# Performance work log

Measured on AMD Instinct MI355X. Metric: run time of the kernel, lower is better.

Reference implementation:

```python
import jax, jax.numpy as jnp
import numpy as np

B, N, C = 16, 32768, 3
PRE, POST, IOU_THRESH = 4096, 512, 0.7


def setup_inputs() -> dict:
    key = jax.random.key(0)
    k1, k2, k3, k4 = jax.random.split(key, 4)
    centers = jax.random.uniform(k1, (B, N, 3), minval=0.0, maxval=70.0)
    sizes = jax.random.uniform(k2, (B, N, 3), minval=1.0, maxval=5.0)
    ry = jax.random.uniform(k3, (B, N, 1), minval=-np.pi, maxval=np.pi)
    batch_box_preds = jnp.concatenate([centers, sizes, ry], axis=-1)  # (B,N,7)
    batch_cls_preds = jax.random.uniform(k4, (B, N, C))  # normalized class scores
    return {"batch_box_preds": batch_box_preds, "batch_cls_preds": batch_cls_preds}


def _nms_single(boxes, scores):
    """Greedy class-agnostic NMS for one sample.
    boxes: (N,7) [x,y,z,dx,dy,dz,ry]; scores: (N,).
    Returns selected indices into the original N boxes and a validity mask,
    both of fixed length POST (padded).
    BEV IoU uses axis-aligned footprints (x,y,dx,dy)."""
    top_s, top_i = jax.lax.top_k(scores, PRE)  # pre-maxsize filtering by score
    tb = boxes[top_i]  # (PRE,7)
    x1 = tb[:, 0] - tb[:, 3] * 0.5
    x2 = tb[:, 0] + tb[:, 3] * 0.5
    y1 = tb[:, 1] - tb[:, 4] * 0.5
    y2 = tb[:, 1] + tb[:, 4] * 0.5
    area = (x2 - x1) * (y2 - y1)

    def step(active, _):
        ms = jnp.where(active, top_s, -jnp.inf)
        j = jnp.argmax(ms)
        valid = active[j]
        ix = jnp.clip(jnp.minimum(x2, x2[j]) - jnp.maximum(x1, x1[j]), 0.0)
        iy = jnp.clip(jnp.minimum(y2, y2[j]) - jnp.maximum(y1, y1[j]), 0.0)
        inter = ix * iy
        iou = inter / (area + area[j] - inter + 1e-8)
        # suppress overlapping boxes (j suppresses itself, iou==1)
        active = active & jnp.where(valid, iou < IOU_THRESH, True)
        return active, (jnp.where(valid, top_i[j], 0), valid)

    active0 = jnp.ones(PRE, dtype=bool)
    _, (sel_idx, sel_valid) = jax.lax.scan(step, active0, None, length=POST)
    return sel_idx, sel_valid


def reference(batch_box_preds, batch_cls_preds):
    # cur_roi_scores, cur_roi_labels = torch.max(cls_preds, dim=1)
    scores = jnp.max(batch_cls_preds, axis=-1)          # (B,N)
    labels = jnp.argmax(batch_cls_preds, axis=-1)       # (B,N)
    sel_idx, sel_valid = jax.vmap(_nms_single)(batch_box_preds, scores)  # (B,POST)
    gather = jax.vmap(lambda a, i: a[i])
    rois = jnp.where(sel_valid[..., None], gather(batch_box_preds, sel_idx), 0.0)  # (B,POST,7)
    roi_scores = jnp.where(sel_valid, gather(scores, sel_idx), 0.0)                # (B,POST)
    roi_labels = jnp.where(sel_valid, gather(labels, sel_idx), 0) + 1              # (B,POST), pad -> 1 as in torch code
    return rois, roi_scores, roi_labels
```

## Files before the change

### kernel.cpp

```cpp
#include <hip/hip_runtime.h>
#include <stdint.h>

#define BATCH 16
#define NBOX  32768
#define PRE   4096
#define POST  512

#define PADIDX(i) ((i) + ((i) >> 4))

typedef unsigned long long u64;
typedef unsigned int u32;

__device__ inline u64 shfl64(u64 v, int src) {
    int lo = __shfl((int)(v & 0xffffffffULL), src);
    int hi = __shfl((int)(v >> 32), src);
    return ((u64)(u32)hi << 32) | (u32)lo;
}

__global__ __launch_bounds__(1024) void k_sortkeys4096(const float* __restrict__ cls,
                                                       u64* __restrict__ out) {
    __shared__ u64 s[PRE + (PRE >> 4)];
    int g = blockIdx.x;
    u64* dst = out + (size_t)g * PRE;
    int tid = threadIdx.x;
    for (int i = tid; i < PRE; i += 1024) {
        int idx = g * PRE + i;
        const float* c = cls + (size_t)idx * 3;
        float sc = fmaxf(fmaxf(c[0], c[1]), c[2]);
        u32 sb = __float_as_uint(sc);
        s[PADIDX(i)] = ((u64)(~sb) << 32) | (u32)(idx & (NBOX - 1));
    }
    for (int k = 2; k <= PRE; k <<= 1) {
        for (int jj = k >> 1; jj > 0; jj >>= 1) {
            __syncthreads();
            for (int p = tid; p < PRE / 2; p += 1024) {
                int i = 2 * p - (p & (jj - 1));
                int l = i + jj;
                bool asc = ((i & k) == 0);
                u64 a = s[PADIDX(i)], b = s[PADIDX(l)];
                if ((a > b) == asc) { s[PADIDX(i)] = b; s[PADIDX(l)] = a; }
            }
        }
    }
    __syncthreads();
    for (int i = tid; i < PRE; i += 1024) dst[i] = s[PADIDX(i)];
}

__global__ __launch_bounds__(256) void k_mergepath(const u64* __restrict__ in,
                                                   u64* __restrict__ out, int npairs) {
    __shared__ u64 sA[PRE], sB[PRE];
    int b = blockIdx.x / npairs, p = blockIdx.x % npairs;
    const u64* A  = in + ((size_t)b * npairs * 2 + (size_t)p * 2) * PRE;
    const u64* Bp = A + PRE;
    u64* dst = out + ((size_t)b * npairs + p) * PRE;
    int tid = threadIdx.x;
    for (int i = tid; i < PRE; i += 256) { sA[i] = A[i]; sB[i] = Bp[i]; }
    __syncthreads();
    int d = tid * 16;
    int lo = d > PRE ? d - PRE : 0;
    int hi = d < PRE ? d : PRE;
    while (lo < hi) {
        int mid = (lo + hi) >> 1;
        if (sA[mid] < sB[d - 1 - mid]) lo = mid + 1; else hi = mid;
    }
    int a = lo, bi = d - lo;
    u64 av = a  < PRE ? sA[a]  : ~0ULL;
    u64 bv = bi < PRE ? sB[bi] : ~0ULL;
    u64 res[16];
    #pragma unroll
    for (int q = 0; q < 16; ++q) {
        bool ta = av < bv;
        res[q] = ta ? av : bv;
        if (ta) { ++a;  av = a  < PRE ? sA[a]  : ~0ULL; }
        else    { ++bi; bv = bi < PRE ? sB[bi] : ~0ULL; }
    }
    #pragma unroll
    for (int q = 0; q < 16; ++q) dst[d + q] = res[q];
}

__global__ __launch_bounds__(256) void k_coords(const u64* __restrict__ topkeys,
                                                const float* __restrict__ boxes,
                                                float* __restrict__ cx1,
                                                float* __restrict__ cy1,
                                                float* __restrict__ cx2,
                                                float* __restrict__ cy2,
                                                float* __restrict__ car,
                                                u64* __restrict__ flags) {
    int g = blockIdx.x * 256 + threadIdx.x;
    if (g < BATCH * 64) flags[g] = 0ULL;
    int b = g >> 12;
    u64 key = topkeys[g];
    int n = (int)(key & 0xffffffffULL);
    const float* bp = boxes + ((size_t)b * NBOX + n) * 7;
    float cx = bp[0], cy = bp[1], dx = bp[3], dy = bp[4];
    float hx = __fmul_rn(dx, 0.5f), hy = __fmul_rn(dy, 0.5f);
    float x1 = __fsub_rn(cx, hx), x2 = __fadd_rn(cx, hx);
    float y1 = __fsub_rn(cy, hy), y2 = __fadd_rn(cy, hy);
    cx1[g] = x1; cy1[g] = y1; cx2[g] = x2; cy2[g] = y2;
    car[g] = __fmul_rn(__fsub_rn(x2, x1), __fsub_rn(y2, y1));
}

__global__ __launch_bounds__(256) void k_iou(const float* __restrict__ cx1,
                                             const float* __restrict__ cy1,
                                             const float* __restrict__ cx2,
                                             const float* __restrict__ cy2,
                                             const float* __restrict__ car,
                                             u64* __restrict__ maskp,
                                             u64* __restrict__ flags) {
    __shared__ float s1[64], s2[64], s3[64], s4[64], s5[64];
    int b = blockIdx.y;
    int t = blockIdx.x, blk = 0;
    while (t >= 64 - blk) { t -= 64 - blk; ++blk; }
    int wd = blk + t;
    bool diag = (wd == blk);
    size_t base = (size_t)b * PRE;
    int tid = threadIdx.x;
    if (tid < 64) {
        int i = blk * 64 + tid;
        s1[tid] = cx1[base + i]; s2[tid] = cy1[base + i];
        s3[tid] = cx2[base + i]; s4[tid] = cy2[base + i];
        s5[tid] = car[base + i];
    }
    __syncthreads();
    int w = tid >> 6, lane = tid & 63;
    int j = wd * 64 + lane;
    float jx1 = cx1[base + j], jy1 = cy1[base + j];
    float jx2 = cx2[base + j], jy2 = cy2[base + j];
    float ja  = car[base + j];
    const double M = (double)0.7f - 0x1p-25;
    u64 wavebits = 0;
    int r0 = w * 16;
    #pragma unroll 4
    for (int r = 0; r < 16; ++r) {
        int i = blk * 64 + r0 + r;
        float rx1 = s1[r0 + r], ry1 = s2[r0 + r];
        float rx2 = s3[r0 + r], ry2 = s4[r0 + r], ra = s5[r0 + r];
        float ix = fmaxf(__fsub_rn(fminf(jx2, rx2), fmaxf(jx1, rx1)), 0.0f);
        float iy = fmaxf(__fsub_rn(fminf(jy2, ry2), fmaxf(jy1, ry1)), 0.0f);
        float inter = __fmul_rn(ix, iy);
        bool cand = (inter > 0.0f) && (!diag || j > i);
        u64 m = 0;
        if (__ballot(cand)) {
            float ssum = __fadd_rn(ja, ra);
            float d    = __fsub_rn(ssum, inter);
            float q    = __fadd_rn(d, 1e-8f);
            bool sup = cand && ((double)inter > M * (double)q);
            m = __ballot(sup);
        }
        if (lane == 0) maskp[((base + i) << 6) + wd] = m;
        if (m) wavebits |= 1ULL << (r0 + r);
    }
    if (lane == 0 && wavebits)
        atomicOr((unsigned long long*)&flags[b * 64 + blk], wavebits);
}

__global__ __launch_bounds__(256) void k_walk(const u64* __restrict__ maskp,
                                              const u64* __restrict__ flagbits,
                                              const u64* __restrict__ topkeys,
                                              const float* __restrict__ boxes,
                                              const float* __restrict__ cls,
                                              float* __restrict__ out) {
    __shared__ int ssel[POST];
    __shared__ int scnt;
    int b = blockIdx.x;
    int tid = threadIdx.x;
    const u64* keys = topkeys + (size_t)b * PRE;

    if (tid < 64) {
        int lane = tid;
        u64 act = ~0ULL;
        u64 nzf = flagbits[b * 64 + lane];
        int cnt = 0;
        while (true) {
            u64 bal = __ballot(act != 0ULL);
            if (!bal) break;
            int fw = __ffsll(bal) - 1;
            u64 wsel = shfl64(act, fw);
            int i = (fw << 6) + __ffsll(wsel) - 1;
            if (lane == 0) ssel[cnt] = i;
            cnt++;
            if (cnt == POST) break;
            if (lane == fw) act &= ~(1ULL << (i & 63));
            u64 fword = shfl64(nzf, fw);
            if ((fword >> (i & 63)) & 1ULL) {
                u64 row = maskp[(((size_t)b * PRE + i) << 6) + lane];
                if (lane >= fw) act &= ~row;
            }
        }
        if (lane == 0) scnt = cnt;
    }
    __syncthreads();
    int cnt = scnt;
    for (int k = tid; k < POST; k += 256) if (k >= cnt) ssel[k] = -1;
    __syncthreads();

    const int R1 = BATCH * POST * 7;
    const int R2 = R1 + BATCH * POST;
    for (int k = tid; k < POST; k += 256) {
        int j = ssel[k];
        float* ro = out + ((size_t)b * POST + k) * 7;
        float score = 0.0f, labelf = 1.0f;
        if (j >= 0) {
            u64 key = keys[j];
            int n = (int)(key & 0xffffffffULL);
            const float* bp = boxes + ((size_t)b * NBOX + n) * 7;
            #pragma unroll
            for (int c = 0; c < 7; ++c) ro[c] = bp[c];
            score = __uint_as_float(~(u32)(key >> 32));
            const float* cp = cls + ((size_t)b * NBOX + n) * 3;
            float c0 = cp[0], c1 = cp[1], c2 = cp[2];
            int lab = 0; float best = c0;
            if (c1 > best) { best = c1; lab = 1; }
            if (c2 > best) { lab = 2; }
            labelf = (float)(lab + 1);
        } else {
            #pragma unroll
            for (int c = 0; c < 7; ++c) ro[c] = 0.0f;
        }
        out[R1 + b * POST + k] = score;
        out[R2 + b * POST + k] = labelf;
    }
}

__global__ __launch_bounds__(1024) void k_nms(const u64* __restrict__ topkeys,
                                              const float* __restrict__ boxes,
                                              const float* __restrict__ cls,
                                              float* __restrict__ out) {
    __shared__ float sx1[PRE], sy1[PRE], sx2[PRE], sy2[PRE], sarea[PRE];
    __shared__ int   sorig[PRE];
    __shared__ u64   smask[PRE / 64];
    __shared__ int   ssel[POST];
    __shared__ int   scur;
    int b = blockIdx.x;
    int tid = threadIdx.x;
    const u64* keys = topkeys + (size_t)b * PRE;

    for (int i = tid; i < PRE; i += 1024) {
        u64 key = keys[i];
        int n = (int)(key & 0xffffffffULL);
        sorig[i] = n;
        const float* bp = boxes + ((size_t)b * NBOX + n) * 7;
        float cx = bp[0], cy = bp[1], dx = bp[3], dy = bp[4];
        float hx = __fmul_rn(dx, 0.5f), hy = __fmul_rn(dy, 0.5f);
        float x1 = __fsub_rn(cx, hx), x2 = __fadd_rn(cx, hx);
        float y1 = __fsub_rn(cy, hy), y2 = __fadd_rn(cy, hy);
        sx1[i] = x1; sx2[i] = x2; sy1[i] = y1; sy2[i] = y2;
        sarea[i] = __fmul_rn(__fsub_rn(x2, x1), __fsub_rn(y2, y1));
    }
    if (tid < PRE / 64) smask[tid] = ~0ULL;
    __syncthreads();

    int lane = tid & 63;
    int wv   = tid >> 6;
    for (int r = 0; r < POST; ++r) {
        if (tid < 64) {
            u64 w = smask[lane];
            u64 nz = __ballot(w != 0ULL);
            int j = -1;
            if (nz) {
                int fw = __ffsll(nz) - 1;
                u64 wf = shfl64(w, fw);
                j = (fw << 6) + __ffsll(wf) - 1;
            }
            if (lane == 0) { scur = j; ssel[r] = j; }
        }
        __syncthreads();
        int j = scur;
        if (j < 0) {
            for (int k = r + tid; k < POST; k += 1024) ssel[k] = -1;
            __syncthreads();
            break;
        }
        float x1j = sx1[j], x2j = sx2[j], y1j = sy1[j], y2j = sy2[j], aj = sarea[j];
        for (int wd = wv * 4; wd < wv * 4 + 4; ++wd) {
            u64 m = smask[wd];
            if (m == 0ULL) continue;
            int i = (wd << 6) + lane;
            float ix = fmaxf(__fsub_rn(fminf(sx2[i], x2j), fmaxf(sx1[i], x1j)), 0.0f);
            float iy = fmaxf(__fsub_rn(fminf(sy2[i], y2j), fmaxf(sy1[i], y1j)), 0.0f);
            float inter = __fmul_rn(ix, iy);
            float denom = __fadd_rn(__fsub_rn(__fadd_rn(sarea[i], aj), inter), 1e-8f);
            float iou = __fdiv_rn(inter, denom);
            u64 clr = __ballot(!(iou < 0.7f));
            if (lane == 0) smask[wd] = m & ~clr;
        }
        __syncthreads();
    }

    const int R1 = BATCH * POST * 7;
    const int R2 = R1 + BATCH * POST;
    for (int k = tid; k < POST; k += 1024) {
        int j = ssel[k];
        float* ro = out + ((size_t)b * POST + k) * 7;
        float score = 0.0f, labelf = 1.0f;
        if (j >= 0) {
            int n = sorig[j];
            const float* bp = boxes + ((size_t)b * NBOX + n) * 7;
            #pragma unroll
            for (int c = 0; c < 7; ++c) ro[c] = bp[c];
            u64 key = keys[j];
            score = __uint_as_float(~(u32)(key >> 32));
            const float* cp = cls + ((size_t)b * NBOX + n) * 3;
            float c0 = cp[0], c1 = cp[1], c2 = cp[2];
            int lab = 0; float best = c0;
            if (c1 > best) { best = c1; lab = 1; }
            if (c2 > best) { lab = 2; }
            labelf = (float)(lab + 1);
        } else {
            #pragma unroll
            for (int c = 0; c < 7; ++c) ro[c] = 0.0f;
        }
        out[R1 + b * POST + k] = score;
        out[R2 + b * POST + k] = labelf;
    }
}

extern "C" void kernel_launch(void* const* d_in, const int* in_sizes, int n_in,
                              void* d_out, int out_size, void* d_ws, size_t ws_size,
                              hipStream_t stream) {
    const float* boxes = (const float*)d_in[0];
    const float* cls   = (const float*)d_in[1];
    float* out = (float*)d_out;

    char* ws = (char*)d_ws;
    u64*   keysA = (u64*)(ws + 0);
    u64*   keysB = (u64*)(ws + 4194304);
    float* cx1   = (float*)(ws + 8388608);
    float* cy1   = (float*)(ws + 8650752);
    float* cx2   = (float*)(ws + 8912896);
    float* cy2   = (float*)(ws + 9175040);
    float* car   = (float*)(ws + 9437184);
    u64*   flags = (u64*)(ws + 9699328);
    u64*   maskp = (u64*)(ws + 9707520);
    const size_t NEED = 9707520 + (size_t)BATCH * PRE * 64 * 8;

    k_sortkeys4096<<<BATCH * 8, 1024, 0, stream>>>(cls, keysB);
    k_mergepath<<<BATCH * 4, 256, 0, stream>>>(keysB, keysA, 4);
    k_mergepath<<<BATCH * 2, 256, 0, stream>>>(keysA, keysB, 2);
    k_mergepath<<<BATCH, 256, 0, stream>>>(keysB, keysA, 1);

    if (ws_size >= NEED) {
        k_coords<<<(BATCH * PRE) / 256, 256, 0, stream>>>(keysA, boxes,
                                                          cx1, cy1, cx2, cy2, car, flags);
        k_iou<<<dim3(2080, BATCH), 256, 0, stream>>>(cx1, cy1, cx2, cy2, car,
                                                     maskp, flags);
        k_walk<<<BATCH, 256, 0, stream>>>(maskp, flags, keysA, boxes, cls, out);
    } else {
        k_nms<<<BATCH, 1024, 0, stream>>>(keysA, boxes, cls, out);
    }
}
```

Measured before the change: 328.3 us.

## Replace dense NMS suppression bitmask with sparse per-row adjacency lists

The IoU kernel no longer writes a dense 64-word bitmask row per box. It appends each suppressed index to a compact per-box list of up to 7 u16 entries, with a global spill buffer for overflow, using atomics. The walk kernel loads these lists into shared memory and rebuilds each lane's 64-bit suppression word from them. This cuts the 32 MB mask write and the dependent global reads in the serial walk. In exchange it adds atomic contention, a memset, a large shared-memory footprint, and a linear spill scan for rows with many overlaps.

Result: faster. 310.6 us (-5.4%).

```diff
diff --git a/kernel.cpp b/kernel.cpp
--- a/kernel.cpp
+++ b/kernel.cpp
@@ -10,6 +10,7 @@
 
 typedef unsigned long long u64;
 typedef unsigned int u32;
+typedef unsigned short u16;
 
 __device__ inline u64 shfl64(u64 v, int src) {
     int lo = __shfl((int)(v & 0xffffffffULL), src);
@@ -84,10 +85,8 @@
                                                 float* __restrict__ cy1,
                                                 float* __restrict__ cx2,
                                                 float* __restrict__ cy2,
-                                                float* __restrict__ car,
-                                                u64* __restrict__ flags) {
+                                                float* __restrict__ car) {
     int g = blockIdx.x * 256 + threadIdx.x;
-    if (g < BATCH * 64) flags[g] = 0ULL;
     int b = g >> 12;
     u64 key = topkeys[g];
     int n = (int)(key & 0xffffffffULL);
@@ -105,15 +104,17 @@
                                              const float* __restrict__ cx2,
                                              const float* __restrict__ cy2,
                                              const float* __restrict__ car,
-                                             u64* __restrict__ maskp,
-                                             u64* __restrict__ flags) {
+                                             u32* __restrict__ counts,
+                                             u16* __restrict__ lists,
+                                             u32* __restrict__ spcnt,
+                                             u32* __restrict__ spill) {
     __shared__ float s1[64], s2[64], s3[64], s4[64], s5[64];
     int b = blockIdx.y;
     int t = blockIdx.x, blk = 0;
     while (t >= 64 - blk) { t -= 64 - blk; ++blk; }
     int wd = blk + t;
-    bool diag = (wd == blk);
     size_t base = (size_t)b * PRE;
+    int bb = b * PRE;
     int tid = threadIdx.x;
     if (tid < 64) {
         int i = blk * 64 + tid;
@@ -128,7 +129,6 @@
     float jx2 = cx2[base + j], jy2 = cy2[base + j];
     float ja  = car[base + j];
     const double M = (double)0.7f - 0x1p-25;
-    u64 wavebits = 0;
     int r0 = w * 16;
     #pragma unroll 4
     for (int r = 0; r < 16; ++r) {
@@ -138,7 +138,7 @@
         float ix = fmaxf(__fsub_rn(fminf(jx2, rx2), fmaxf(jx1, rx1)), 0.0f);
         float iy = fmaxf(__fsub_rn(fminf(jy2, ry2), fmaxf(jy1, ry1)), 0.0f);
         float inter = __fmul_rn(ix, iy);
-        bool cand = (inter > 0.0f) && (!diag || j > i);
+        bool cand = (j > i) && (inter > 0.0f);
         u64 m = 0;
         if (__ballot(cand)) {
             float ssum = __fadd_rn(ja, ra);
@@ -147,29 +147,59 @@
             bool sup = cand && ((double)inter > M * (double)q);
             m = __ballot(sup);
         }
-        if (lane == 0) maskp[((base + i) << 6) + wd] = m;
-        if (m) wavebits |= 1ULL << (r0 + r);
-    }
-    if (lane == 0 && wavebits)
-        atomicOr((unsigned long long*)&flags[b * 64 + blk], wavebits);
-}
-
-__global__ __launch_bounds__(256) void k_walk(const u64* __restrict__ maskp,
-                                              const u64* __restrict__ flagbits,
+        if (lane == 0 && m) {
+            u64 mm = m;
+            while (mm) {
+                int jj = __ffsll(mm) - 1; mm &= mm - 1;
+                u32 slot = atomicAdd(&counts[bb + i], 1u);
+                if (slot < 7)
+                    lists[((size_t)(bb + i)) * 8 + 1 + slot] = (u16)(wd * 64 + jj);
+                else {
+                    u32 sp = atomicAdd(&spcnt[b], 1u);
+                    if (sp < 4096) spill[(b << 12) + sp] = ((u32)i << 16) | (u32)(wd * 64 + jj);
+                }
+            }
+        }
+    }
+}
+
+__global__ __launch_bounds__(256) void k_walk(const u32* __restrict__ counts,
+                                              const u16* __restrict__ lists,
+                                              const u32* __restrict__ spcnt,
+                                              const u32* __restrict__ spill,
                                               const u64* __restrict__ topkeys,
                                               const float* __restrict__ boxes,
                                               const float* __restrict__ cls,
                                               float* __restrict__ out) {
-    __shared__ int ssel[POST];
-    __shared__ int scnt;
+    __shared__ uint4 lrow[PRE];
+    __shared__ u32   lbits[128];
+    __shared__ u32   lspill[4096];
+    __shared__ int   ssel[POST];
+    __shared__ int   scnt, ssp;
     int b = blockIdx.x;
     int tid = threadIdx.x;
     const u64* keys = topkeys + (size_t)b * PRE;
+    const uint4* listv = (const uint4*)(lists + ((size_t)b * PRE) * 8);
+
+    if (tid < 128) lbits[tid] = 0;
+    if (tid == 0) { u32 s = spcnt[b]; ssp = s > 4096u ? 4096 : (int)s; }
+    __syncthreads();
+    for (int i = tid; i < PRE; i += 256) {
+        uint4 row = listv[i];
+        u32 c = counts[b * PRE + i];
+        row.x = (row.x & 0xFFFF0000u) | (c > 65535u ? 65535u : c);
+        lrow[i] = row;
+        if (c) atomicOr(&lbits[i >> 5], 1u << (i & 31));
+    }
+    __syncthreads();
+    int spn = ssp;
+    for (int q = tid; q < spn; q += 256) lspill[q] = spill[(b << 12) + q];
+    __syncthreads();
 
     if (tid < 64) {
         int lane = tid;
         u64 act = ~0ULL;
-        u64 nzf = flagbits[b * 64 + lane];
+        u64 hasl = ((u64)lbits[2 * lane + 1] << 32) | lbits[2 * lane];
         int cnt = 0;
         while (true) {
             u64 bal = __ballot(act != 0ULL);
@@ -178,13 +208,31 @@
             u64 wsel = shfl64(act, fw);
             int i = (fw << 6) + __ffsll(wsel) - 1;
             if (lane == 0) ssel[cnt] = i;
-            cnt++;
-            if (cnt == POST) break;
+            if (++cnt == POST) break;
             if (lane == fw) act &= ~(1ULL << (i & 63));
-            u64 fword = shfl64(nzf, fw);
-            if ((fword >> (i & 63)) & 1ULL) {
-                u64 row = maskp[(((size_t)b * PRE + i) << 6) + lane];
-                if (lane >= fw) act &= ~row;
+            u64 hb = shfl64(hasl, fw);
+            if ((hb >> (i & 63)) & 1ULL) {
+                uint4 row = lrow[i];
+                int c = (int)(row.x & 0xFFFFu);
+                u64 m = 0;
+                int e;
+                e = (int)(row.x >> 16);      if (c > 0 && (e >> 6) == lane) m |= 1ULL << (e & 63);
+                e = (int)(row.y & 0xFFFFu);  if (c > 1 && (e >> 6) == lane) m |= 1ULL << (e & 63);
+                e = (int)(row.y >> 16);      if (c > 2 && (e >> 6) == lane) m |= 1ULL << (e & 63);
+                e = (int)(row.z & 0xFFFFu);  if (c > 3 && (e >> 6) == lane) m |= 1ULL << (e & 63);
+                e = (int)(row.z >> 16);      if (c > 4 && (e >> 6) == lane) m |= 1ULL << (e & 63);
+                e = (int)(row.w & 0xFFFFu);  if (c > 5 && (e >> 6) == lane) m |= 1ULL << (e & 63);
+                e = (int)(row.w >> 16);      if (c > 6 && (e >> 6) == lane) m |= 1ULL << (e & 63);
+                if (c > 7) {
+                    for (int q = 0; q < spn; ++q) {
+                        u32 en = lspill[q];
+                        if ((int)(en >> 16) == i) {
+                            int j2 = (int)(en & 0xFFFFu);
+                            if ((j2 >> 6) == lane) m |= 1ULL << (j2 & 63);
+                        }
+                    }
+                }
+                act &= ~m;
             }
         }
         if (lane == 0) scnt = cnt;
@@ -323,16 +371,18 @@
     float* out = (float*)d_out;
 
     char* ws = (char*)d_ws;
-    u64*   keysA = (u64*)(ws + 0);
-    u64*   keysB = (u64*)(ws + 4194304);
-    float* cx1   = (float*)(ws + 8388608);
-    float* cy1   = (float*)(ws + 8650752);
-    float* cx2   = (float*)(ws + 8912896);
-    float* cy2   = (float*)(ws + 9175040);
-    float* car   = (float*)(ws + 9437184);
-    u64*   flags = (u64*)(ws + 9699328);
-    u64*   maskp = (u64*)(ws + 9707520);
-    const size_t NEED = 9707520 + (size_t)BATCH * PRE * 64 * 8;
+    u64*   keysA  = (u64*)(ws + 0);
+    u64*   keysB  = (u64*)(ws + 4194304);
+    float* cx1    = (float*)(ws + 8388608);
+    float* cy1    = (float*)(ws + 8650752);
+    float* cx2    = (float*)(ws + 8912896);
+    float* cy2    = (float*)(ws + 9175040);
+    float* car    = (float*)(ws + 9437184);
+    u32*   counts = (u32*)(ws + 9699328);
+    u32*   spcnt  = (u32*)(ws + 9961472);
+    u32*   spill  = (u32*)(ws + 9961536);
+    u16*   lists  = (u16*)(ws + 10223680);
+    const size_t NEED = 10223680 + (size_t)BATCH * PRE * 8 * sizeof(u16);
 
     k_sortkeys4096<<<BATCH * 8, 1024, 0, stream>>>(cls, keysB);
     k_mergepath<<<BATCH * 4, 256, 0, stream>>>(keysB, keysA, 4);
@@ -340,11 +390,13 @@
     k_mergepath<<<BATCH, 256, 0, stream>>>(keysB, keysA, 1);
 
     if (ws_size >= NEED) {
+        hipMemsetAsync(ws + 9699328, 0, 262208, stream);
         k_coords<<<(BATCH * PRE) / 256, 256, 0, stream>>>(keysA, boxes,
-                                                          cx1, cy1, cx2, cy2, car, flags);
+                                                          cx1, cy1, cx2, cy2, car);
         k_iou<<<dim3(2080, BATCH), 256, 0, stream>>>(cx1, cy1, cx2, cy2, car,
-                                                     maskp, flags);
-        k_walk<<<BATCH, 256, 0, stream>>>(maskp, flags, keysA, boxes, cls, out);
+                                                     counts, lists, spcnt, spill);
+        k_walk<<<BATCH, 256, 0, stream>>>(counts, lists, spcnt, spill,
+                                          keysA, boxes, cls, out);
     } else {
         k_nms<<<BATCH, 1024, 0, stream>>>(keysA, boxes, cls, out);
     }
```
